# Kernel tuning notes

Hardware: AMD Instinct MI355X
Metric: run time of the kernel (lower is better)

## Reference

```python
import jax, jax.numpy as jnp
import numpy as np

B, H, W, CIN, C, L = 2, 512, 512, 64, 64, 4
TAU = 1.0


def _conv3x3(x, w):
    # NHWC input, HWIO kernel, SAME zero padding, stride 1 (SignalConv2D corr=True)
    return jax.lax.conv_general_dilated(
        x, w, window_strides=(1, 1), padding='SAME',
        dimension_numbers=('NHWC', 'HWIO', 'NHWC'))


def setup_inputs() -> dict:
    key = jax.random.key(0)
    ks = jax.random.split(key, 10)
    return {
        'x0': jax.random.normal(ks[0], (B, H, W, CIN), jnp.float32),
        'spa_mask': jax.random.uniform(ks[1], (B, H, W, 1), jnp.float32),
        'gumbel_u': jax.random.uniform(ks[2], (1, L, 2, C), jnp.float32),
        'ch_mask': jax.random.uniform(ks[3], (1, L, 2, C), jnp.float32),
        'w0': jax.random.normal(ks[4], (3, 3, CIN, C), jnp.float32) * 0.05,
        'w1': jax.random.normal(ks[5], (3, 3, C, C), jnp.float32) * 0.05,
        'w2': jax.random.normal(ks[6], (3, 3, C, C), jnp.float32) * 0.05,
        'w3': jax.random.normal(ks[7], (3, 3, C, C), jnp.float32) * 0.05,
        'w_collect': jax.random.normal(ks[8], (L * C, C), jnp.float32) * 0.05,
        'b_collect': jnp.zeros((C,), jnp.float32),
    }


def reference(x0, spa_mask, gumbel_u, ch_mask, w0, w1, w2, w3, w_collect, b_collect):
    # Gumbel-softmax channel routing mask over the {dense, sparse} axis (axis=2)
    g = -jnp.log(-jnp.log(jnp.clip(gumbel_u, 1e-10, 1.0)))
    ch = jax.nn.softmax((ch_mask + g) / TAU, axis=2)  # (1, L, 2, C)

    ws = [w0, w1, w2, w3]
    out_feats = []
    fea = x0
    for i in range(L):
        cd = ch[:, i, 0, :][:, None, None, :]  # dense-channel mask  (1,1,1,C)
        cs = ch[:, i, 1, :][:, None, None, :]  # sparse-channel mask (1,1,1,C)
        if i == 0:
            fea = _conv3x3(fea, ws[0])
            fea = fea * cs * spa_mask + fea * cd
        else:
            cdp = ch[:, i - 1, 0, :][:, None, None, :]
            csp = ch[:, i - 1, 1, :][:, None, None, :]
            fea_d = _conv3x3(fea * cdp, ws[i])
            fea_s = _conv3x3(fea * csp, ws[i])
            fea = (fea_d * cs * spa_mask + fea_d * cd
                   + fea_s * cs * spa_mask + fea_s * cd * spa_mask)
        fea = jax.nn.relu(fea)
        out_feats.append(fea)

    cat = jnp.concatenate(out_feats, axis=-1)  # (B, H, W, L*C)
    # 1x1 stride-1 Conv2DTranspose == pointwise linear + bias
    out = jnp.einsum('bhwi,io->bhwo', cat, w_collect) + b_collect
    return out, ch
```

## Files before the change

kernel.cpp:

```cpp
#include <hip/hip_runtime.h>
#include <hip/hip_fp16.h>

#define BB 2
#define HH 512
#define WW 512
#define CC 64
#define PW 514
#define PIMG (514*514)

typedef _Float16 f16;
typedef _Float16 f16x8 __attribute__((ext_vector_type(8)));
typedef _Float16 f16x4 __attribute__((ext_vector_type(4)));
typedef float f32x4 __attribute__((ext_vector_type(4)));

static __device__ __forceinline__ f16x8 zero_f16x8() {
    f16x8 z = {(f16)0,(f16)0,(f16)0,(f16)0,(f16)0,(f16)0,(f16)0,(f16)0};
    return z;
}

__global__ void k_prep_ch(const float* __restrict__ gum, const float* __restrict__ chm,
                          float* __restrict__ ws_ch, float* __restrict__ out_ch) {
    int t = threadIdx.x;
    int l = t >> 6, c = t & 63;
    float u0 = gum[(l*2+0)*64+c], u1 = gum[(l*2+1)*64+c];
    u0 = fminf(fmaxf(u0, 1e-10f), 1.0f);
    u1 = fminf(fmaxf(u1, 1e-10f), 1.0f);
    float a0 = chm[(l*2+0)*64+c] - logf(-logf(u0));
    float a1 = chm[(l*2+1)*64+c] - logf(-logf(u1));
    float m = fmaxf(a0, a1);
    float e0 = expf(a0-m), e1 = expf(a1-m);
    float s = e0 + e1;
    float c0 = e0/s, c1 = e1/s;
    ws_ch[(l*2+0)*64+c] = c0;  ws_ch[(l*2+1)*64+c] = c1;
    out_ch[(l*2+0)*64+c] = c0; out_ch[(l*2+1)*64+c] = c1;
}

__global__ void k_pack(const float* __restrict__ w0, const float* __restrict__ w1,
                       const float* __restrict__ w2, const float* __restrict__ w3,
                       const float* __restrict__ wc, const float* __restrict__ ch,
                       f16* __restrict__ bpk0, f16* __restrict__ bpkL, f16* __restrict__ wcpk) {
    int idx = blockIdx.x * 256 + threadIdx.x;
    if (idx < 36864) {
        int j = idx & 7, lane = (idx>>3)&63, nb = (idx>>9)&3, kb = idx>>11;
        int k = kb*32 + (lane>>4)*8 + j;
        int tap = k>>6, ci = k&63;
        int co = nb*16 + (lane&15);
        bpk0[idx] = (f16)w0[(tap*64+ci)*64+co];
    } else if (idx < 36864 + 221184) {
        int i2 = idx - 36864;
        int l = i2 / 73728;
        int r = i2 % 73728;
        int j = r&7, lane=(r>>3)&63, nb=(r>>9)&7, kb=r>>12;
        int k = kb*32 + (lane>>4)*8 + j;
        int tap = k>>6, ci = k&63;
        int copr = nb*16 + (lane&15);
        int co = copr & 63;
        const float* w = (l==0)? w1 : (l==1)? w2 : w3;
        float scale = (copr < 64) ? ch[(l*2+0)*64+ci] : ch[(l*2+1)*64+ci];
        bpkL[i2] = (f16)(w[(tap*64+ci)*64+co] * scale);
    } else if (idx < 36864 + 221184 + 16384) {
        int i3 = idx - (36864 + 221184);
        int j=i3&7, lane=(i3>>3)&63, nb=(i3>>9)&3, kb=(i3>>11)&1, l=i3>>12;
        int k = kb*32 + (lane>>4)*8 + j;
        int n = nb*16 + (lane&15);
        wcpk[i3] = (f16)wc[(l*64+k)*64+n];
    }
}

__global__ void k_guard(f16* __restrict__ buf) {
    int idx = blockIdx.x*256 + threadIdx.x;
    const int TOT = 2*2052*8;
    if (idx >= TOT) return;
    int c8 = idx & 7, g = idx >> 3;
    int b = g / 2052, r = g % 2052;
    int hp, wp;
    if      (r < 514)  { hp = 0;        wp = r; }
    else if (r < 1028) { hp = 513;      wp = r-514; }
    else if (r < 1540) { hp = r-1027;   wp = 0; }
    else               { hp = r-1539;   wp = 513; }
    *(f16x8*)(buf + ((size_t)(b*PW+hp)*PW + wp)*64 + c8*8) = zero_f16x8();
}

template<int MODE>
__global__ __launch_bounds__(256, 2) void k_conv(const void* __restrict__ in_, f16* __restrict__ out,
        const f16* __restrict__ bpk, const float* __restrict__ ch_l,
        const float* __restrict__ spa) {
    constexpr int NBT = (MODE==0) ? 4 : 8;
    constexpr int NF  = (MODE==0) ? 2 : 4;
    __shared__ f16 smem[4*136*64];
    const int wt = blockIdx.x, hb = blockIdx.y, b = blockIdx.z;
    const int h0 = hb*2;
    const int tid = threadIdx.x, lane = tid & 63, wid = tid >> 6;
    const int px0 = wt*128;
    const int sub  = lane & 7;
    const int srel = lane >> 3;
    const int cblk = sub ^ srel;

    if (MODE == 0) {
        const float* inF = (const float*)in_;
        #pragma unroll
        for (int half = 0; half < 2; ++half) {
            const int J0 = half ? 9 : 0;
            const int JN = half ? 8 : 9;
            f32x4 v0[9], v1[9];
            bool ok[9];
            int dst[9];
            #pragma unroll
            for (int t = 0; t < JN; ++t) {
                int j = (J0 + t)*4 + wid;
                int r = j / 17, i = j % 17;
                int s = i*8 + srel;
                int hin = h0 + r - 1;
                int win = px0 + s - 1;
                ok[t] = ((unsigned)hin < HH) && ((unsigned)win < WW);
                dst[t] = r*17408 + i*1024 + lane*16;
                if (ok[t]) {
                    const f32x4* p = (const f32x4*)(inF + (((size_t)(b*HH + hin)*WW + win)*CC + cblk*8));
                    v0[t] = p[0];
                    v1[t] = p[1];
                }
            }
            #pragma unroll
            for (int t = 0; t < JN; ++t) {
                f16x8 o = zero_f16x8();
                if (ok[t]) {
                    o[0]=(f16)v0[t][0]; o[1]=(f16)v0[t][1]; o[2]=(f16)v0[t][2]; o[3]=(f16)v0[t][3];
                    o[4]=(f16)v1[t][0]; o[5]=(f16)v1[t][1]; o[6]=(f16)v1[t][2]; o[7]=(f16)v1[t][3];
                }
                *(f16x8*)((char*)smem + dst[t]) = o;
            }
        }
        __syncthreads();
    } else {
        const f16* inH = (const f16*)in_;
        #pragma unroll
        for (int jj = 0; jj < 9; ++jj) {
            int j = jj*4 + wid;
            if (j < 34) {
                int r = j / 17, i = j % 17;
                int s = i*8 + srel;
                const f16* src = inH + ((size_t)(b*PW + h0 + r)*PW + (px0 + s))*64 + cblk*8;
                __builtin_amdgcn_global_load_lds(
                    (const __attribute__((address_space(1))) uint32_t*)src,
                    (__attribute__((address_space(3))) uint32_t*)
                        ((char*)smem + r*17408 + i*1024),
                    16, 0, 0);
            }
        }
        __syncthreads();
        #pragma unroll
        for (int jj = 0; jj < 9; ++jj) {
            int j = 34 + jj*4 + wid;
            if (j < 68) {
                int r = j / 17, i = j % 17;
                int s = i*8 + srel;
                const f16* src = inH + ((size_t)(b*PW + h0 + r)*PW + (px0 + s))*64 + cblk*8;
                __builtin_amdgcn_global_load_lds(
                    (const __attribute__((address_space(1))) uint32_t*)src,
                    (__attribute__((address_space(3))) uint32_t*)
                        ((char*)smem + r*17408 + i*1024),
                    16, 0, 0);
            }
        }
    }

    const int wr = wid >> 1, wn = wid & 1;
    const int lrow = lane & 15, q = lane >> 4;
    const char* smw = (const char*)smem + wr*17408;

    int sb[8][3], po[2][3];
    #pragma unroll
    for (int dxi = 0; dxi < 3; ++dxi) {
        int m7 = (lrow + dxi) & 7;
        po[0][dxi] = ((q)     ^ m7) * 16;
        po[1][dxi] = ((4 + q) ^ m7) * 16;
        #pragma unroll
        for (int mf = 0; mf < 8; ++mf)
            sb[mf][dxi] = (mf*16 + lrow + dxi) * 128;
    }

    f32x4 acc[8][NF];
    #pragma unroll
    for (int i=0;i<8;i++)
        #pragma unroll
        for (int j=0;j<NF;j++) { f32x4 z = {0.f,0.f,0.f,0.f}; acc[i][j] = z; }

    int nbIdx[4];
    nbIdx[0]=wn*2; nbIdx[1]=wn*2+1; nbIdx[2]=wn*2+4; nbIdx[3]=wn*2+5;

    const f16* blane = bpk + (size_t)lane*8;

    f16x8 acur[8], anxt[8], bcur[NF], bnxt[NF];
    #pragma unroll
    for (int nf=0; nf<NF; ++nf)
        bcur[nf] = *reinterpret_cast<const f16x8*>(blane + (size_t)nbIdx[nf]*512);
    #pragma unroll
    for (int mf=0; mf<8; ++mf)
        acur[mf] = *(const f16x8*)(smw + sb[mf][0] + po[0][0]);

    #pragma unroll
    for (int kb = 0; kb < 18; ++kb) {
        if (MODE == 1 && kb == 5) __syncthreads();
        if (kb < 17) {
            const int kn = kb + 1;
            const int rn = kn/6, dxin = (kn%6)/2, halfn = kn & 1;
            #pragma unroll
            for (int nf=0; nf<NF; ++nf)
                bnxt[nf] = *reinterpret_cast<const f16x8*>(blane + (size_t)(kn*NBT + nbIdx[nf])*512);
            #pragma unroll
            for (int mf=0; mf<8; ++mf)
                anxt[mf] = *(const f16x8*)(smw + rn*17408 + sb[mf][dxin] + po[halfn][dxin]);
        }
        __builtin_amdgcn_s_setprio(1);
        #pragma unroll
        for (int nf=0; nf<NF; ++nf) {
            #pragma unroll
            for (int mf=0; mf<8; ++mf)
                acc[mf][nf] = __builtin_amdgcn_mfma_f32_16x16x32_f16(acur[mf], bcur[nf], acc[mf][nf], 0,0,0);
        }
        __builtin_amdgcn_s_setprio(0);
        #pragma unroll
        for (int nf=0; nf<NF; ++nf) bcur[nf] = bnxt[nf];
        #pragma unroll
        for (int mf=0; mf<8; ++mf) acur[mf] = anxt[mf];
    }

    const float* cd = ch_l;
    const float* cs = ch_l + 64;
    const int h = h0 + wr;
    const size_t sparow = (size_t)(b*HH + h)*WW;
    const size_t outrow = (size_t)(b*PW + h + 1)*PW + 1;
    #pragma unroll
    for (int mf=0; mf<8; ++mf) {
        const int pixb = mf*16 + q*4;
        f32x4 sp4 = *(const f32x4*)(spa + sparow + px0 + pixb);
        float sp[4] = {sp4[0], sp4[1], sp4[2], sp4[3]};
        #pragma unroll
        for (int nf2=0; nf2<2; ++nf2) {
            int co = wn*32 + nf2*16 + lrow;
            float vcd = cd[co], vcs = cs[co];
            #pragma unroll
            for (int r=0; r<4; ++r) {
                float v;
                if (MODE==0) v = acc[mf][nf2][r] * (vcs*sp[r] + vcd);
                else         v = acc[mf][nf2][r] * (vcs*sp[r] + vcd) + acc[mf][nf2+2][r] * sp[r];
                v = fmaxf(v, 0.f);
                out[(outrow + px0 + pixb + r)*64 + co] = (f16)v;
            }
        }
    }
}

__global__ __launch_bounds__(256) void k_collect_all(
        const f16* __restrict__ f0, const f16* __restrict__ f1,
        const f16* __restrict__ f2, const f16* __restrict__ f3,
        const f16* __restrict__ wcpk, const float* __restrict__ bias,
        float* __restrict__ out) {
    const int wt = blockIdx.x, h = blockIdx.y, b = blockIdx.z;
    const int tid = threadIdx.x;
    const int lane = tid & 63, wid = tid >> 6;
    const int lrow = lane & 15, lk = (lane>>4)*8;
    const size_t inrow  = (size_t)(b*PW + h + 1)*PW + 1;
    const size_t outrow = (size_t)(b*HH + h)*WW;
    const int px0 = wt*256 + wid*64;

    const f16* feas[4] = {f0, f1, f2, f3};

    f32x4 acc[4][4];
    #pragma unroll
    for (int i=0;i<4;i++)
        #pragma unroll
        for (int j=0;j<4;j++) { f32x4 z = {0.f,0.f,0.f,0.f}; acc[i][j] = z; }

    #pragma unroll
    for (int kb=0; kb<8; ++kb) {
        const f16* fl = feas[kb>>1];
        f16x8 a[4];
        #pragma unroll
        for (int mf=0; mf<4; ++mf)
            a[mf] = *reinterpret_cast<const f16x8*>(fl + (inrow + px0 + mf*16 + lrow)*64 + (kb&1)*32 + lk);
        #pragma unroll
        for (int nf=0; nf<4; ++nf) {
            f16x8 bb = *reinterpret_cast<const f16x8*>(wcpk + ((size_t)(kb*4 + nf)*64 + lane)*8);
            #pragma unroll
            for (int mf=0; mf<4; ++mf)
                acc[mf][nf] = __builtin_amdgcn_mfma_f32_16x16x32_f16(bb, a[mf], acc[mf][nf], 0,0,0);
        }
    }
    const int q = lane >> 4;
    #pragma unroll
    for (int mf=0; mf<4; ++mf) {
        const int pix = px0 + mf*16 + lrow;
        float* orow = out + (outrow + pix)*CC;
        #pragma unroll
        for (int nf=0; nf<4; ++nf) {
            const int co0 = nf*16 + q*4;
            f32x4 b4 = *(const f32x4*)(bias + co0);
            *(f32x4*)(orow + co0) = acc[mf][nf] + b4;
        }
    }
}

template<bool FIRST>
__global__ __launch_bounds__(256) void k_collect(const f16* __restrict__ fea,
        const f16* __restrict__ wcpk_l, const float* __restrict__ bias,
        float* __restrict__ out) {
    const int wt = blockIdx.x, h = blockIdx.y, b = blockIdx.z;
    const int tid = threadIdx.x;
    const int lane = tid & 63, wid = tid >> 6;
    const int lrow = lane & 15, lk = (lane>>4)*8;
    const size_t inrow  = (size_t)(b*PW + h + 1)*PW + 1;
    const size_t outrow = (size_t)(b*HH + h)*WW;
    const int px0 = wt*64 + wid*16;

    f32x4 acc[4];
    #pragma unroll
    for (int j=0;j<4;j++) { f32x4 z = {0.f,0.f,0.f,0.f}; acc[j] = z; }

    #pragma unroll
    for (int kb=0; kb<2; ++kb) {
        f16x8 a = *reinterpret_cast<const f16x8*>(fea + (inrow + px0 + lrow)*64 + kb*32 + lk);
        #pragma unroll
        for (int nf=0; nf<4; ++nf) {
            f16x8 bb = *reinterpret_cast<const f16x8*>(wcpk_l + ((size_t)(kb*4 + nf)*64 + lane)*8);
            acc[nf] = __builtin_amdgcn_mfma_f32_16x16x32_f16(bb, a, acc[nf], 0,0,0);
        }
    }
    const int q = lane >> 4;
    const int pix = px0 + lrow;
    float* orow = out + (outrow + pix)*CC;
    #pragma unroll
    for (int nf=0; nf<4; ++nf) {
        const int co0 = nf*16 + q*4;
        f32x4 v = acc[nf];
        #pragma unroll
        for (int r=0;r<4;++r) {
            float x = v[r];
            if (FIRST) x += bias[co0+r];
            else       x += orow[co0+r];
            orow[co0+r] = x;
        }
    }
}

extern "C" void kernel_launch(void* const* d_in, const int* in_sizes, int n_in,
                              void* d_out, int out_size, void* d_ws, size_t ws_size,
                              hipStream_t stream) {
    const float* x0  = (const float*)d_in[0];
    const float* spa = (const float*)d_in[1];
    const float* gum = (const float*)d_in[2];
    const float* chm = (const float*)d_in[3];
    const float* w0  = (const float*)d_in[4];
    const float* w1  = (const float*)d_in[5];
    const float* w2  = (const float*)d_in[6];
    const float* w3  = (const float*)d_in[7];
    const float* wc  = (const float*)d_in[8];
    const float* bias= (const float*)d_in[9];
    float* out = (float*)d_out;

    char* ws = (char*)d_ws;
    const size_t WBASE = (1u<<20);
    const size_t FB = 67699712ull;
    const size_t NEED_A = WBASE + 4*FB;
    const size_t NEED_B = WBASE + 2*FB;
    if (ws_size < NEED_B) return;

    float* ws_ch = (float*)ws;
    f16* bpk0 = (f16*)(ws + 4096);
    f16* bpkL = (f16*)(ws + 4096 + 73728);
    f16* wcpk = (f16*)(ws + 4096 + 73728 + 442368);

    k_prep_ch<<<1, 256, 0, stream>>>(gum, chm, ws_ch, out + 33554432);
    k_pack<<<1072, 256, 0, stream>>>(w0, w1, w2, w3, wc, ws_ch, bpk0, bpkL, wcpk);

    dim3 gcv(4, 256, 2);
    dim3 gca(2, 512, 2);
    dim3 gcf(8, 512, 2);

    if (ws_size >= NEED_A) {
        f16* R0 = (f16*)(ws + WBASE);
        f16* R1 = (f16*)(ws + WBASE + FB);
        f16* R2 = (f16*)(ws + WBASE + 2*FB);
        f16* R3 = (f16*)(ws + WBASE + 3*FB);
        k_guard<<<129, 256, 0, stream>>>(R1);
        k_guard<<<129, 256, 0, stream>>>(R2);
        k_guard<<<129, 256, 0, stream>>>(R3);
        k_conv<0><<<gcv, 256, 0, stream>>>(x0, R1, bpk0,          ws_ch + 0,   spa);
        k_conv<1><<<gcv, 256, 0, stream>>>(R1, R2, bpkL + 0,      ws_ch + 128, spa);
        k_conv<1><<<gcv, 256, 0, stream>>>(R2, R3, bpkL + 73728,  ws_ch + 256, spa);
        k_conv<1><<<gcv, 256, 0, stream>>>(R3, R0, bpkL + 147456, ws_ch + 384, spa);
        k_collect_all<<<gca, 256, 0, stream>>>(R1, R2, R3, R0, wcpk, bias, out);
    } else {
        f16* P0 = (f16*)(ws + WBASE);
        f16* P1 = (f16*)(ws + WBASE + FB);
        k_guard<<<129, 256, 0, stream>>>(P0);
        k_guard<<<129, 256, 0, stream>>>(P1);
        k_conv<0><<<gcv, 256, 0, stream>>>(x0, P1, bpk0,          ws_ch + 0,   spa);
        k_collect<true ><<<gcf, 256, 0, stream>>>(P1, wcpk + 0,     bias, out);
        k_conv<1><<<gcv, 256, 0, stream>>>(P1, P0, bpkL + 0,      ws_ch + 128, spa);
        k_collect<false><<<gcf, 256, 0, stream>>>(P0, wcpk + 4096,  bias, out);
        k_conv<1><<<gcv, 256, 0, stream>>>(P0, P1, bpkL + 73728,  ws_ch + 256, spa);
        k_collect<false><<<gcf, 256, 0, stream>>>(P1, wcpk + 8192,  bias, out);
        k_conv<1><<<gcv, 256, 0, stream>>>(P1, P0, bpkL + 147456, ws_ch + 384, spa);
        k_collect<false><<<gcf, 256, 0, stream>>>(P0, wcpk + 12288, bias, out);
    }
}
```

Baseline: 356.4 us.

## Overlap second-half fp32 input staging with MFMA in first conv layer

The first (fp32-input) conv layer used to load and convert all four halo rows to LDS before any math. It now loads rows 0-1 and issues the global loads for rows 2-3 up front, stores only the first half, and starts MFMAs. The second half is converted and written to LDS at kb==5, followed by a barrier, mirroring the MODE 1 split. This hides global load latency behind compute but keeps 72 extra float4 registers live across the early MFMA loop, which risks spills or lower occupancy. The final fp32 output stores in the collect path also become nontemporal.

Result: slower. 385.4 us (+8.1%).

```diff
diff --git a/kernel.cpp b/kernel.cpp
--- a/kernel.cpp
+++ b/kernel.cpp
@@ -96,38 +96,62 @@
     const int srel = lane >> 3;
     const int cblk = sub ^ srel;
 
+    f32x4 v0b[9], v1b[9];
+    bool okb[9];
+    int dstb[9];
+
     if (MODE == 0) {
         const float* inF = (const float*)in_;
-        #pragma unroll
-        for (int half = 0; half < 2; ++half) {
-            const int J0 = half ? 9 : 0;
-            const int JN = half ? 8 : 9;
-            f32x4 v0[9], v1[9];
-            bool ok[9];
-            int dst[9];
-            #pragma unroll
-            for (int t = 0; t < JN; ++t) {
-                int j = (J0 + t)*4 + wid;
+        f32x4 v0a[9], v1a[9];
+        bool oka[9];
+        int dsta[9];
+        #pragma unroll
+        for (int t = 0; t < 9; ++t) {
+            int j = t*4 + wid;
+            oka[t] = false;
+            if (j < 34) {
                 int r = j / 17, i = j % 17;
                 int s = i*8 + srel;
-                int hin = h0 + r - 1;
-                int win = px0 + s - 1;
-                ok[t] = ((unsigned)hin < HH) && ((unsigned)win < WW);
-                dst[t] = r*17408 + i*1024 + lane*16;
-                if (ok[t]) {
+                int hin = h0 + r - 1, win = px0 + s - 1;
+                bool ok = ((unsigned)hin < HH) && ((unsigned)win < WW);
+                oka[t] = ok;
+                dsta[t] = r*17408 + i*1024 + lane*16;
+                if (ok) {
                     const f32x4* p = (const f32x4*)(inF + (((size_t)(b*HH + hin)*WW + win)*CC + cblk*8));
-                    v0[t] = p[0];
-                    v1[t] = p[1];
+                    v0a[t] = p[0];
+                    v1a[t] = p[1];
                 }
             }
-            #pragma unroll
-            for (int t = 0; t < JN; ++t) {
+        }
+        #pragma unroll
+        for (int t = 0; t < 9; ++t) {
+            int jj = t*4 + wid;
+            okb[t] = false;
+            dstb[t] = -1;
+            if (jj < 34) {
+                int j = 34 + jj;
+                int r = j / 17, i = j % 17;
+                int s = i*8 + srel;
+                int hin = h0 + r - 1, win = px0 + s - 1;
+                bool ok = ((unsigned)hin < HH) && ((unsigned)win < WW);
+                okb[t] = ok;
+                dstb[t] = r*17408 + i*1024 + lane*16;
+                if (ok) {
+                    const f32x4* p = (const f32x4*)(inF + (((size_t)(b*HH + hin)*WW + win)*CC + cblk*8));
+                    v0b[t] = p[0];
+                    v1b[t] = p[1];
+                }
+            }
+        }
+        #pragma unroll
+        for (int t = 0; t < 9; ++t) {
+            if (t*4 + wid < 34) {
                 f16x8 o = zero_f16x8();
-                if (ok[t]) {
-                    o[0]=(f16)v0[t][0]; o[1]=(f16)v0[t][1]; o[2]=(f16)v0[t][2]; o[3]=(f16)v0[t][3];
-                    o[4]=(f16)v1[t][0]; o[5]=(f16)v1[t][1]; o[6]=(f16)v1[t][2]; o[7]=(f16)v1[t][3];
+                if (oka[t]) {
+                    o[0]=(f16)v0a[t][0]; o[1]=(f16)v0a[t][1]; o[2]=(f16)v0a[t][2]; o[3]=(f16)v0a[t][3];
+                    o[4]=(f16)v1a[t][0]; o[5]=(f16)v1a[t][1]; o[6]=(f16)v1a[t][2]; o[7]=(f16)v1a[t][3];
                 }
-                *(f16x8*)((char*)smem + dst[t]) = o;
+                *(f16x8*)((char*)smem + dsta[t]) = o;
             }
         }
         __syncthreads();
@@ -200,7 +224,22 @@
 
     #pragma unroll
     for (int kb = 0; kb < 18; ++kb) {
-        if (MODE == 1 && kb == 5) __syncthreads();
+        if (kb == 5) {
+            if (MODE == 0) {
+                #pragma unroll
+                for (int t = 0; t < 9; ++t) {
+                    if (t*4 + wid < 34) {
+                        f16x8 o = zero_f16x8();
+                        if (okb[t]) {
+                            o[0]=(f16)v0b[t][0]; o[1]=(f16)v0b[t][1]; o[2]=(f16)v0b[t][2]; o[3]=(f16)v0b[t][3];
+                            o[4]=(f16)v1b[t][0]; o[5]=(f16)v1b[t][1]; o[6]=(f16)v1b[t][2]; o[7]=(f16)v1b[t][3];
+                        }
+                        *(f16x8*)((char*)smem + dstb[t]) = o;
+                    }
+                }
+            }
+            __syncthreads();
+        }
         if (kb < 17) {
             const int kn = kb + 1;
             const int rn = kn/6, dxin = (kn%6)/2, halfn = kn & 1;
@@ -296,7 +335,8 @@
         for (int nf=0; nf<4; ++nf) {
             const int co0 = nf*16 + q*4;
             f32x4 b4 = *(const f32x4*)(bias + co0);
-            *(f32x4*)(orow + co0) = acc[mf][nf] + b4;
+            f32x4 v = acc[mf][nf] + b4;
+            __builtin_nontemporal_store(v, (f32x4*)(orow + co0));
         }
     }
 }
```
